# Kernel tuning notes

Hardware: AMD Instinct MI355X
Metric: run time of the kernel (lower is better)

Reference implementation:

```python
import jax, jax.numpy as jnp
import numpy as np

NEG_SLOPE = 0.2
EPS = 1e-16
HEADS1, OUT1 = 4, 32
HEADS2, OUT2 = 1, 32


def _gat_conv(x, W, a_src, a_dst, bias, src, dst, num_nodes, heads, out_c, concat):
    # x: [N, F_in], W: [F_in, heads*out_c], a_*: [heads, out_c]
    h = (x @ W).reshape(num_nodes, heads, out_c)            # [N, H, C]
    alpha_src = (h * a_src).sum(-1)                          # [N, H]
    alpha_dst = (h * a_dst).sum(-1)                          # [N, H]
    e = jax.nn.leaky_relu(alpha_src[src] + alpha_dst[dst], NEG_SLOPE)  # [E, H]
    # softmax over incoming edges of each destination node (PyG softmax)
    m = jax.ops.segment_max(e, dst, num_segments=num_nodes)
    ex = jnp.exp(e - m[dst])
    s = jax.ops.segment_sum(ex, dst, num_segments=num_nodes)
    alpha = ex / (s[dst] + EPS)                              # [E, H]
    out = jax.ops.segment_sum(h[src] * alpha[:, :, None], dst,
                              num_segments=num_nodes)        # [N, H, C]
    out = out.reshape(num_nodes, heads * out_c) if concat else out.mean(axis=1)
    return out + bias


def setup_inputs() -> dict:
    key = jax.random.key(0)
    ks = jax.random.split(key, 10)
    N, E, F_IN = 50000, 1600000, 128
    sc = 0.1
    return {
        "x": jax.random.normal(ks[0], (N, F_IN), jnp.float32),
        "edge_index": jax.random.randint(ks[1], (2, E), 0, N, jnp.int32),
        "W1": jax.random.normal(ks[2], (F_IN, HEADS1 * OUT1), jnp.float32) * sc,
        "a_src1": jax.random.normal(ks[3], (HEADS1, OUT1), jnp.float32) * sc,
        "a_dst1": jax.random.normal(ks[4], (HEADS1, OUT1), jnp.float32) * sc,
        "b1": jax.random.normal(ks[5], (HEADS1 * OUT1,), jnp.float32) * sc,
        "W2": jax.random.normal(ks[6], (HEADS1 * OUT1, HEADS2 * OUT2), jnp.float32) * sc,
        "a_src2": jax.random.normal(ks[7], (HEADS2, OUT2), jnp.float32) * sc,
        "a_dst2": jax.random.normal(ks[8], (HEADS2, OUT2), jnp.float32) * sc,
        "b2": jax.random.normal(ks[9], (OUT2,), jnp.float32) * sc,
    }


def reference(x, edge_index, W1, a_src1, a_dst1, b1, W2, a_src2, a_dst2, b2):
    N = x.shape[0]
    # PyG GATConv default add_self_loops=True
    loops = jnp.arange(N, dtype=edge_index.dtype)
    src = jnp.concatenate([edge_index[0], loops])
    dst = jnp.concatenate([edge_index[1], loops])
    h = _gat_conv(x, W1, a_src1, a_dst1, b1, src, dst, N, HEADS1, OUT1, True)
    h = jax.nn.elu(h)
    return _gat_conv(h, W2, a_src2, a_dst2, b2, src, dst, N, HEADS2, OUT2, False)
```

## Files before the change

### kernel.cpp

```cpp
#include <hip/hip_runtime.h>
#include <math.h>

#define NEG_SLOPE 0.2f
#define EPSV 1e-16f
#define NPART 16

typedef _Float16 half4 __attribute__((ext_vector_type(4)));
typedef _Float16 half8 __attribute__((ext_vector_type(8)));


__global__ void k_hist_rank(const int* __restrict__ ei, int E, int ET, int N,
                            int* __restrict__ degp, int* __restrict__ rank){
    int i = blockIdx.x * 256 + threadIdx.x;
    if (i < ET){
        int d = (i < E) ? ei[E + i] : (i - E);
        int p = blockIdx.x & (NPART - 1);
        rank[i] = atomicAdd(&degp[p * N + d], 1);
    }
}

__global__ void k_combine(const int* __restrict__ degp, int N,
                          int* __restrict__ deg, int* __restrict__ poff){
    int n = blockIdx.x * 256 + threadIdx.x;
    if (n < N){
        int s = 0;
        #pragma unroll
        for (int p = 0; p < NPART; p++){
            int t = degp[p * N + n];
            poff[p * N + n] = s;
            s += t;
        }
        deg[n] = s;
    }
}

__global__ void k_scan_blk(const int* __restrict__ deg, int N,
                           int* __restrict__ rowptr, int* __restrict__ bsum){
    int b = blockIdx.x, t = threadIdx.x;
    int base = b * 1024 + t * 4;
    int v[4];
    #pragma unroll
    for (int j = 0; j < 4; j++) v[j] = (base + j < N) ? deg[base + j] : 0;
    int s = v[0] + v[1] + v[2] + v[3];
    int lane = t & 63, wid = t >> 6;
    int x = s;
    #pragma unroll
    for (int off = 1; off < 64; off <<= 1){
        int y = __shfl_up(x, off, 64);
        if (lane >= off) x += y;
    }
    __shared__ int ws[4];
    if (lane == 63) ws[wid] = x;
    __syncthreads();
    int woff = 0;
    for (int w = 0; w < wid; w++) woff += ws[w];
    int run = woff + x - s;
    #pragma unroll
    for (int j = 0; j < 4; j++){
        if (base + j < N) rowptr[base + j] = run;
        run += v[j];
    }
    if (t == 255) bsum[b] = woff + x;
}

__global__ void k_scan_top(int* bsum, int nb){
    int t = threadIdx.x;
    int v = (t < nb) ? bsum[t] : 0;
    int x = v;
    #pragma unroll
    for (int off = 1; off < 64; off <<= 1){
        int y = __shfl_up(x, off, 64);
        if (t >= off) x += y;
    }
    if (t < nb) bsum[t] = x - v;
}

__global__ void k_finalize(const int* __restrict__ bsum, int N, int ET,
                           int* __restrict__ rowptr, int* __restrict__ poff){
    int n = blockIdx.x * 256 + threadIdx.x;
    if (n < N){
        int r = rowptr[n] + bsum[n >> 10];
        rowptr[n] = r;
        #pragma unroll
        for (int p = 0; p < NPART; p++) poff[p * N + n] += r;
    }
    if (n == 0) rowptr[N] = ET;
}

__launch_bounds__(256)
__global__ void k_scatter2(const int* __restrict__ ei, int E, int ET, int N,
                           const int* __restrict__ poff, const int* __restrict__ rank,
                           int* __restrict__ csr_src){
    int i = blockIdx.x * 256 + threadIdx.x;
    if (i >= ET) return;
    int s, d;
    if (i < E){ s = ei[i]; d = ei[E + i]; } else { s = i - E; d = s; }
    int p = blockIdx.x & (NPART - 1);
    csr_src[poff[p * N + d] + rank[i]] = s;
}


__launch_bounds__(256)
__global__ void k_gemm1(const float* __restrict__ x, const float* __restrict__ W1,
                        const float* __restrict__ a_src, const float* __restrict__ a_dst,
                        _Float16* __restrict__ h1h, float* __restrict__ asrc1,
                        float* __restrict__ adst1, int N){
    __shared__ float Wl[128 * 128];
    __shared__ float xl[32 * 128];
    int t = threadIdx.x;
    int cg = t & 31, ns = t >> 5;
    for (int idx = t; idx < 4096; idx += 256)
        *(float4*)&Wl[idx * 4] = *(const float4*)&W1[idx * 4];
    int n0 = blockIdx.x * 32;
    for (int idx = t; idx < 1024; idx += 256){
        int row = idx >> 5, k4 = idx & 31;
        float4 v = {0.f, 0.f, 0.f, 0.f};
        if (n0 + row < N) v = *(const float4*)&x[(size_t)(n0 + row) * 128 + k4 * 4];
        *(float4*)&xl[row * 128 + k4 * 4] = v;
    }
    __syncthreads();
    float4 acc0 = {0,0,0,0}, acc1 = {0,0,0,0}, acc2 = {0,0,0,0}, acc3 = {0,0,0,0};
    #pragma unroll 4
    for (int k = 0; k < 128; k++){
        float4 w = *(float4*)&Wl[k * 128 + cg * 4];
        float x0 = xl[(ns     ) * 128 + k];
        float x1 = xl[(ns +  8) * 128 + k];
        float x2v= xl[(ns + 16) * 128 + k];
        float x3 = xl[(ns + 24) * 128 + k];
        acc0.x = fmaf(x0, w.x, acc0.x); acc0.y = fmaf(x0, w.y, acc0.y);
        acc0.z = fmaf(x0, w.z, acc0.z); acc0.w = fmaf(x0, w.w, acc0.w);
        acc1.x = fmaf(x1, w.x, acc1.x); acc1.y = fmaf(x1, w.y, acc1.y);
        acc1.z = fmaf(x1, w.z, acc1.z); acc1.w = fmaf(x1, w.w, acc1.w);
        acc2.x = fmaf(x2v, w.x, acc2.x); acc2.y = fmaf(x2v, w.y, acc2.y);
        acc2.z = fmaf(x2v, w.z, acc2.z); acc2.w = fmaf(x2v, w.w, acc2.w);
        acc3.x = fmaf(x3, w.x, acc3.x); acc3.y = fmaf(x3, w.y, acc3.y);
        acc3.z = fmaf(x3, w.z, acc3.z); acc3.w = fmaf(x3, w.w, acc3.w);
    }
    float4 a4s = *(const float4*)&a_src[cg * 4];
    float4 a4d = *(const float4*)&a_dst[cg * 4];
    float4 accs[4] = {acc0, acc1, acc2, acc3};
    #pragma unroll
    for (int j = 0; j < 4; j++){
        int n = n0 + ns + 8 * j;
        if (n >= N) continue;
        float4 a = accs[j];
        half4 hv;
        hv.x = (_Float16)a.x; hv.y = (_Float16)a.y;
        hv.z = (_Float16)a.z; hv.w = (_Float16)a.w;
        *(half4*)&h1h[((size_t)n << 7) + (cg << 2)] = hv;
        float vs = a.x * a4s.x + a.y * a4s.y + a.z * a4s.z + a.w * a4s.w;
        float vd = a.x * a4d.x + a.y * a4d.y + a.z * a4d.z + a.w * a4d.w;
        #pragma unroll
        for (int m = 1; m <= 4; m <<= 1){
            vs += __shfl_xor(vs, m, 64);
            vd += __shfl_xor(vd, m, 64);
        }
        if ((cg & 7) == 0){
            int head = cg >> 3;
            asrc1[n * 4 + head] = vs;
            adst1[n * 4 + head] = vd;
        }
    }
}


__launch_bounds__(256)
__global__ void k_agg1(const int* __restrict__ rowptr, const int* __restrict__ csr_src,
                       const float* __restrict__ asrc1, const float* __restrict__ adst1,
                       const _Float16* __restrict__ h1h,
                       const float* __restrict__ b1, float* __restrict__ x2){
    int t = threadIdx.x;
    int n = blockIdx.x * 4 + (t >> 6);
    int lane = t & 63, g = lane >> 4, l = lane & 15, head = l >> 2;
    int start = rowptr[n], end = rowptr[n + 1];
    float adn = adst1[(n << 2) + head];
    float rA[8] = {0,0,0,0,0,0,0,0}, rB[8] = {0,0,0,0,0,0,0,0};
    float sA = 0.f, sB = 0.f;
    int i = start + g;
    for (; i + 4 < end; i += 8){
        int s0 = csr_src[i];
        int s1 = csr_src[i + 4];
        float e0 = asrc1[(s0 << 2) + head] + adn;
        float e1 = asrc1[(s1 << 2) + head] + adn;
        e0 = fmaxf(e0, NEG_SLOPE * e0);
        e1 = fmaxf(e1, NEG_SLOPE * e1);
        float w0 = __expf(e0);
        float w1 = __expf(e1);
        half8 h0 = *(const half8*)&h1h[((size_t)s0 << 7) + (l << 3)];
        half8 h1v = *(const half8*)&h1h[((size_t)s1 << 7) + (l << 3)];
        sA += w0; sB += w1;
        #pragma unroll
        for (int j = 0; j < 8; j++){
            rA[j] = fmaf(w0, (float)h0[j], rA[j]);
            rB[j] = fmaf(w1, (float)h1v[j], rB[j]);
        }
    }
    if (i < end){
        int s0 = csr_src[i];
        float e0 = asrc1[(s0 << 2) + head] + adn;
        e0 = fmaxf(e0, NEG_SLOPE * e0);
        float w0 = __expf(e0);
        half8 h0 = *(const half8*)&h1h[((size_t)s0 << 7) + (l << 3)];
        sA += w0;
        #pragma unroll
        for (int j = 0; j < 8; j++) rA[j] = fmaf(w0, (float)h0[j], rA[j]);
    }
    float r[9];
    #pragma unroll
    for (int j = 0; j < 8; j++) r[j] = rA[j] + rB[j];
    r[8] = sA + sB;
    #pragma unroll
    for (int m = 16; m <= 32; m <<= 1)
        #pragma unroll
        for (int j = 0; j < 9; j++) r[j] += __shfl_xor(r[j], m, 64);
    if (g == 0){
        float inv = 1.f / (r[8] + EPSV);
        float o[8];
        #pragma unroll
        for (int j = 0; j < 8; j++){
            float v = r[j] * inv + b1[l * 8 + j];
            o[j] = (v > 0.f) ? v : expm1f(v);
        }
        float4 o0 = {o[0], o[1], o[2], o[3]};
        float4 o1 = {o[4], o[5], o[6], o[7]};
        *(float4*)&x2[((size_t)n << 7) + (l << 3)]     = o0;
        *(float4*)&x2[((size_t)n << 7) + (l << 3) + 4] = o1;
    }
}


__launch_bounds__(256)
__global__ void k_gemm2(const float* __restrict__ x2, const float* __restrict__ W2,
                        const float* __restrict__ a_src, const float* __restrict__ a_dst,
                        _Float16* __restrict__ h2h, float* __restrict__ asrc2,
                        float* __restrict__ adst2, int N){
    __shared__ float Wl[128 * 32];
    __shared__ float xl[128 * 128];
    int t = threadIdx.x;
    int cg = t & 7, ns = t >> 3;
    for (int idx = t; idx < 1024; idx += 256)
        *(float4*)&Wl[idx * 4] = *(const float4*)&W2[idx * 4];
    int n0 = blockIdx.x * 128;
    for (int idx = t; idx < 4096; idx += 256){
        int row = idx >> 5, k4 = idx & 31;
        float4 v = {0.f, 0.f, 0.f, 0.f};
        if (n0 + row < N) v = *(const float4*)&x2[(size_t)(n0 + row) * 128 + k4 * 4];
        *(float4*)&xl[row * 128 + k4 * 4] = v;
    }
    __syncthreads();
    float4 acc0 = {0,0,0,0}, acc1 = {0,0,0,0}, acc2 = {0,0,0,0}, acc3 = {0,0,0,0};
    #pragma unroll 4
    for (int k = 0; k < 128; k++){
        float4 w = *(float4*)&Wl[k * 32 + cg * 4];
        float x0 = xl[(ns      ) * 128 + k];
        float x1 = xl[(ns +  32) * 128 + k];
        float x2v= xl[(ns +  64) * 128 + k];
        float x3 = xl[(ns +  96) * 128 + k];
        acc0.x = fmaf(x0, w.x, acc0.x); acc0.y = fmaf(x0, w.y, acc0.y);
        acc0.z = fmaf(x0, w.z, acc0.z); acc0.w = fmaf(x0, w.w, acc0.w);
        acc1.x = fmaf(x1, w.x, acc1.x); acc1.y = fmaf(x1, w.y, acc1.y);
        acc1.z = fmaf(x1, w.z, acc1.z); acc1.w = fmaf(x1, w.w, acc1.w);
        acc2.x = fmaf(x2v, w.x, acc2.x); acc2.y = fmaf(x2v, w.y, acc2.y);
        acc2.z = fmaf(x2v, w.z, acc2.z); acc2.w = fmaf(x2v, w.w, acc2.w);
        acc3.x = fmaf(x3, w.x, acc3.x); acc3.y = fmaf(x3, w.y, acc3.y);
        acc3.z = fmaf(x3, w.z, acc3.z); acc3.w = fmaf(x3, w.w, acc3.w);
    }
    float4 a4s = *(const float4*)&a_src[cg * 4];
    float4 a4d = *(const float4*)&a_dst[cg * 4];
    float4 accs[4] = {acc0, acc1, acc2, acc3};
    #pragma unroll
    for (int j = 0; j < 4; j++){
        int n = n0 + ns + 32 * j;
        if (n >= N) continue;
        float4 a = accs[j];
        half4 hv;
        hv.x = (_Float16)a.x; hv.y = (_Float16)a.y;
        hv.z = (_Float16)a.z; hv.w = (_Float16)a.w;
        *(half4*)&h2h[((size_t)n << 5) + (cg << 2)] = hv;
        float vs = a.x * a4s.x + a.y * a4s.y + a.z * a4s.z + a.w * a4s.w;
        float vd = a.x * a4d.x + a.y * a4d.y + a.z * a4d.z + a.w * a4d.w;
        #pragma unroll
        for (int m = 1; m <= 4; m <<= 1){
            vs += __shfl_xor(vs, m, 64);
            vd += __shfl_xor(vd, m, 64);
        }
        if (cg == 0){ asrc2[n] = vs; adst2[n] = vd; }
    }
}


__launch_bounds__(256)
__global__ void k_agg2(const int* __restrict__ rowptr, const int* __restrict__ csr_src,
                       const float* __restrict__ asrc2, const float* __restrict__ adst2,
                       const _Float16* __restrict__ h2h,
                       const float* __restrict__ b2, float* __restrict__ out){
    int t = threadIdx.x;
    int n = blockIdx.x * 4 + (t >> 6);
    int lane = t & 63, g = lane >> 3, l = lane & 7;
    int start = rowptr[n], end = rowptr[n + 1];
    float adn = adst2[n];
    float4 aA = {0,0,0,0}, aB = {0,0,0,0};
    float sA = 0.f, sB = 0.f;
    int i = start + g;
    for (; i + 8 < end; i += 16){
        int s0 = csr_src[i];
        int s1 = csr_src[i + 8];
        float e0 = asrc2[s0] + adn;
        float e1 = asrc2[s1] + adn;
        e0 = fmaxf(e0, NEG_SLOPE * e0);
        e1 = fmaxf(e1, NEG_SLOPE * e1);
        float w0 = __expf(e0);
        float w1 = __expf(e1);
        half4 h0 = *(const half4*)&h2h[((size_t)s0 << 5) + (l << 2)];
        half4 h1v = *(const half4*)&h2h[((size_t)s1 << 5) + (l << 2)];
        sA += w0; sB += w1;
        aA.x = fmaf(w0, (float)h0.x, aA.x); aA.y = fmaf(w0, (float)h0.y, aA.y);
        aA.z = fmaf(w0, (float)h0.z, aA.z); aA.w = fmaf(w0, (float)h0.w, aA.w);
        aB.x = fmaf(w1, (float)h1v.x, aB.x); aB.y = fmaf(w1, (float)h1v.y, aB.y);
        aB.z = fmaf(w1, (float)h1v.z, aB.z); aB.w = fmaf(w1, (float)h1v.w, aB.w);
    }
    if (i < end){
        int s0 = csr_src[i];
        float e0 = asrc2[s0] + adn;
        e0 = fmaxf(e0, NEG_SLOPE * e0);
        float w0 = __expf(e0);
        half4 h0 = *(const half4*)&h2h[((size_t)s0 << 5) + (l << 2)];
        sA += w0;
        aA.x = fmaf(w0, (float)h0.x, aA.x); aA.y = fmaf(w0, (float)h0.y, aA.y);
        aA.z = fmaf(w0, (float)h0.z, aA.z); aA.w = fmaf(w0, (float)h0.w, aA.w);
    }
    float4 acc = {aA.x + aB.x, aA.y + aB.y, aA.z + aB.z, aA.w + aB.w};
    float ssum = sA + sB;
    #pragma unroll
    for (int m = 8; m <= 32; m <<= 1){
        acc.x += __shfl_xor(acc.x, m, 64);
        acc.y += __shfl_xor(acc.y, m, 64);
        acc.z += __shfl_xor(acc.z, m, 64);
        acc.w += __shfl_xor(acc.w, m, 64);
        ssum  += __shfl_xor(ssum,  m, 64);
    }
    if (g == 0){
        float inv = 1.f / (ssum + EPSV);
        const float4 b4 = *(const float4*)&b2[l * 4];
        float4 o;
        o.x = acc.x * inv + b4.x; o.y = acc.y * inv + b4.y;
        o.z = acc.z * inv + b4.z; o.w = acc.w * inv + b4.w;
        *(float4*)&out[((size_t)n << 5) + l * 4] = o;
    }
}


extern "C" void kernel_launch(void* const* d_in, const int* in_sizes, int n_in,
                              void* d_out, int out_size, void* d_ws, size_t ws_size,
                              hipStream_t stream){
    const float* x      = (const float*)d_in[0];
    const int*   ei     = (const int*)  d_in[1];
    const float* W1     = (const float*)d_in[2];
    const float* a_src1 = (const float*)d_in[3];
    const float* a_dst1 = (const float*)d_in[4];
    const float* b1     = (const float*)d_in[5];
    const float* W2     = (const float*)d_in[6];
    const float* a_src2 = (const float*)d_in[7];
    const float* a_dst2 = (const float*)d_in[8];
    const float* b2     = (const float*)d_in[9];
    float* out = (float*)d_out;

    int N  = in_sizes[0] / 128;
    int E  = in_sizes[1] / 2;
    int ET = E + N;
    int nScanBlk = (N + 1023) / 1024;
    int G  = (ET + 255) / 256;

    char* ws = (char*)d_ws;
    size_t off = 0;
    auto alloc = [&](size_t bytes) -> char* {
        char* p = ws + off;
        off += (bytes + 255) & ~(size_t)255;
        return p;
    };
    int*      degp    = (int*)     alloc((size_t)NPART * N * 4);
    int*      deg     = (int*)     alloc((size_t)N * 4);
    int*      rowptr  = (int*)     alloc((size_t)(N + 1) * 4);
    int*      bsum    = (int*)     alloc((size_t)nScanBlk * 4);
    int*      rank    = (int*)     alloc((size_t)ET * 4);
    int*      poff    = (int*)     alloc((size_t)NPART * N * 4);
    int*      csr_src = (int*)     alloc((size_t)ET * 4);
    _Float16* h1h     = (_Float16*)alloc((size_t)N * 128 * 2);
    float*    x2      = (float*)   alloc((size_t)N * 128 * 4);
    float*    asrc1   = (float*)   alloc((size_t)N * 4 * 4);
    float*    adst1   = (float*)   alloc((size_t)N * 4 * 4);
    _Float16* h2h     = (_Float16*)alloc((size_t)N * 32 * 2);
    float*    asrc2   = (float*)   alloc((size_t)N * 4);
    float*    adst2   = (float*)   alloc((size_t)N * 4);

    hipMemsetAsync(degp, 0, (size_t)NPART * N * 4, stream);
    hipLaunchKernelGGL(k_hist_rank, dim3(G), dim3(256), 0, stream, ei, E, ET, N, degp, rank);
    hipLaunchKernelGGL(k_combine,   dim3((N + 255) / 256), dim3(256), 0, stream, degp, N, deg, poff);
    hipLaunchKernelGGL(k_scan_blk,  dim3(nScanBlk), dim3(256), 0, stream, deg, N, rowptr, bsum);
    hipLaunchKernelGGL(k_scan_top,  dim3(1),        dim3(64),  0, stream, bsum, nScanBlk);
    hipLaunchKernelGGL(k_finalize,  dim3((N + 255) / 256), dim3(256), 0, stream, bsum, N, ET, rowptr, poff);
    hipLaunchKernelGGL(k_scatter2,  dim3(G), dim3(256), 0, stream, ei, E, ET, N, poff, rank, csr_src);
    hipLaunchKernelGGL(k_gemm1,     dim3((N + 31) / 32), dim3(256), 0, stream, x, W1, a_src1, a_dst1, h1h, asrc1, adst1, N);
    hipLaunchKernelGGL(k_agg1,      dim3(N / 4), dim3(256), 0, stream, rowptr, csr_src, asrc1, adst1, h1h, b1, x2);
    hipLaunchKernelGGL(k_gemm2,     dim3((N + 127) / 128), dim3(256), 0, stream, x2, W2, a_src2, a_dst2, h2h, asrc2, adst2, N);
    hipLaunchKernelGGL(k_agg2,      dim3(N / 4), dim3(256), 0, stream, rowptr, csr_src, asrc2, adst2, h2h, b2, out);
}
```

Before: 343.4 us.

## Fold CSR scan kernels, vectorize GEMM x loads, deepen aggregation unroll

Merges k_combine and k_scan_top into the scan and finalize kernels, so finalize now recomputes the block-sum prefix and the per-partition offsets directly from degp. This removes two launches and the intermediate deg buffer. Both GEMM inner loops now read x from shared memory as float4 instead of as scalars. Both aggregation kernels now use four independent accumulator streams instead of two, giving more memory-level parallelism on the gathers. The cost is more register pressure and some redundant reads of bsum and degp.

```diff
diff --git a/kernel.cpp b/kernel.cpp
--- a/kernel.cpp
+++ b/kernel.cpp
@@ -19,28 +19,20 @@
     }
 }
 
-__global__ void k_combine(const int* __restrict__ degp, int N,
-                          int* __restrict__ deg, int* __restrict__ poff){
-    int n = blockIdx.x * 256 + threadIdx.x;
-    if (n < N){
-        int s = 0;
-        #pragma unroll
-        for (int p = 0; p < NPART; p++){
-            int t = degp[p * N + n];
-            poff[p * N + n] = s;
-            s += t;
-        }
-        deg[n] = s;
-    }
-}
-
-__global__ void k_scan_blk(const int* __restrict__ deg, int N,
+__global__ void k_scan_blk(const int* __restrict__ degp, int N,
                            int* __restrict__ rowptr, int* __restrict__ bsum){
     int b = blockIdx.x, t = threadIdx.x;
     int base = b * 1024 + t * 4;
     int v[4];
     #pragma unroll
-    for (int j = 0; j < 4; j++) v[j] = (base + j < N) ? deg[base + j] : 0;
+    for (int j = 0; j < 4; j++){
+        int n = base + j, s = 0;
+        if (n < N){
+            #pragma unroll
+            for (int p = 0; p < NPART; p++) s += degp[p * N + n];
+        }
+        v[j] = s;
+    }
     int s = v[0] + v[1] + v[2] + v[3];
     int lane = t & 63, wid = t >> 6;
     int x = s;
@@ -63,26 +55,23 @@
     if (t == 255) bsum[b] = woff + x;
 }
 
-__global__ void k_scan_top(int* bsum, int nb){
-    int t = threadIdx.x;
-    int v = (t < nb) ? bsum[t] : 0;
-    int x = v;
-    #pragma unroll
-    for (int off = 1; off < 64; off <<= 1){
-        int y = __shfl_up(x, off, 64);
-        if (t >= off) x += y;
-    }
-    if (t < nb) bsum[t] = x - v;
-}
-
-__global__ void k_finalize(const int* __restrict__ bsum, int N, int ET,
+__global__ void k_finalize(const int* __restrict__ bsum, const int* __restrict__ degp,
+                           int N, int ET,
                            int* __restrict__ rowptr, int* __restrict__ poff){
-    int n = blockIdx.x * 256 + threadIdx.x;
+    int b = blockIdx.x, t = threadIdx.x;
+    int n = b * 256 + t;
+    int chunk = (b * 256) >> 10;
+    int off = 0;
+    for (int c = 0; c < chunk; c++) off += bsum[c];
     if (n < N){
-        int r = rowptr[n] + bsum[n >> 10];
+        int r = rowptr[n] + off;
         rowptr[n] = r;
-        #pragma unroll
-        for (int p = 0; p < NPART; p++) poff[p * N + n] += r;
+        int run = r;
+        #pragma unroll
+        for (int p = 0; p < NPART; p++){
+            poff[p * N + n] = run;
+            run += degp[p * N + n];
+        }
     }
     if (n == 0) rowptr[N] = ET;
 }
@@ -120,21 +109,28 @@
     }
     __syncthreads();
     float4 acc0 = {0,0,0,0}, acc1 = {0,0,0,0}, acc2 = {0,0,0,0}, acc3 = {0,0,0,0};
-    #pragma unroll 4
-    for (int k = 0; k < 128; k++){
-        float4 w = *(float4*)&Wl[k * 128 + cg * 4];
-        float x0 = xl[(ns     ) * 128 + k];
-        float x1 = xl[(ns +  8) * 128 + k];
-        float x2v= xl[(ns + 16) * 128 + k];
-        float x3 = xl[(ns + 24) * 128 + k];
-        acc0.x = fmaf(x0, w.x, acc0.x); acc0.y = fmaf(x0, w.y, acc0.y);
-        acc0.z = fmaf(x0, w.z, acc0.z); acc0.w = fmaf(x0, w.w, acc0.w);
-        acc1.x = fmaf(x1, w.x, acc1.x); acc1.y = fmaf(x1, w.y, acc1.y);
-        acc1.z = fmaf(x1, w.z, acc1.z); acc1.w = fmaf(x1, w.w, acc1.w);
-        acc2.x = fmaf(x2v, w.x, acc2.x); acc2.y = fmaf(x2v, w.y, acc2.y);
-        acc2.z = fmaf(x2v, w.z, acc2.z); acc2.w = fmaf(x2v, w.w, acc2.w);
-        acc3.x = fmaf(x3, w.x, acc3.x); acc3.y = fmaf(x3, w.y, acc3.y);
-        acc3.z = fmaf(x3, w.z, acc3.z); acc3.w = fmaf(x3, w.w, acc3.w);
+    #pragma unroll 2
+    for (int k = 0; k < 128; k += 4){
+        float4 xv0 = *(float4*)&xl[(ns     ) * 128 + k];
+        float4 xv1 = *(float4*)&xl[(ns +  8) * 128 + k];
+        float4 xv2 = *(float4*)&xl[(ns + 16) * 128 + k];
+        float4 xv3 = *(float4*)&xl[(ns + 24) * 128 + k];
+        #pragma unroll
+        for (int kk = 0; kk < 4; kk++){
+            float4 w = *(float4*)&Wl[(k + kk) * 128 + cg * 4];
+            float x0 = ((float*)&xv0)[kk];
+            float x1 = ((float*)&xv1)[kk];
+            float x2v= ((float*)&xv2)[kk];
+            float x3 = ((float*)&xv3)[kk];
+            acc0.x = fmaf(x0, w.x, acc0.x); acc0.y = fmaf(x0, w.y, acc0.y);
+            acc0.z = fmaf(x0, w.z, acc0.z); acc0.w = fmaf(x0, w.w, acc0.w);
+            acc1.x = fmaf(x1, w.x, acc1.x); acc1.y = fmaf(x1, w.y, acc1.y);
+            acc1.z = fmaf(x1, w.z, acc1.z); acc1.w = fmaf(x1, w.w, acc1.w);
+            acc2.x = fmaf(x2v, w.x, acc2.x); acc2.y = fmaf(x2v, w.y, acc2.y);
+            acc2.z = fmaf(x2v, w.z, acc2.z); acc2.w = fmaf(x2v, w.w, acc2.w);
+            acc3.x = fmaf(x3, w.x, acc3.x); acc3.y = fmaf(x3, w.y, acc3.y);
+            acc3.z = fmaf(x3, w.z, acc3.z); acc3.w = fmaf(x3, w.w, acc3.w);
+        }
     }
     float4 a4s = *(const float4*)&a_src[cg * 4];
     float4 a4d = *(const float4*)&a_dst[cg * 4];
@@ -175,27 +171,35 @@
     int start = rowptr[n], end = rowptr[n + 1];
     float adn = adst1[(n << 2) + head];
     float rA[8] = {0,0,0,0,0,0,0,0}, rB[8] = {0,0,0,0,0,0,0,0};
-    float sA = 0.f, sB = 0.f;
+    float rC[8] = {0,0,0,0,0,0,0,0}, rD[8] = {0,0,0,0,0,0,0,0};
+    float sA = 0.f, sB = 0.f, sC = 0.f, sD = 0.f;
     int i = start + g;
-    for (; i + 4 < end; i += 8){
+    for (; i + 12 < end; i += 16){
         int s0 = csr_src[i];
         int s1 = csr_src[i + 4];
+        int s2 = csr_src[i + 8];
+        int s3 = csr_src[i + 12];
         float e0 = asrc1[(s0 << 2) + head] + adn;
         float e1 = asrc1[(s1 << 2) + head] + adn;
-        e0 = fmaxf(e0, NEG_SLOPE * e0);
-        e1 = fmaxf(e1, NEG_SLOPE * e1);
-        float w0 = __expf(e0);
-        float w1 = __expf(e1);
+        float e2 = asrc1[(s2 << 2) + head] + adn;
+        float e3 = asrc1[(s3 << 2) + head] + adn;
+        e0 = fmaxf(e0, NEG_SLOPE * e0); e1 = fmaxf(e1, NEG_SLOPE * e1);
+        e2 = fmaxf(e2, NEG_SLOPE * e2); e3 = fmaxf(e3, NEG_SLOPE * e3);
+        float w0 = __expf(e0), w1 = __expf(e1), w2 = __expf(e2), w3 = __expf(e3);
         half8 h0 = *(const half8*)&h1h[((size_t)s0 << 7) + (l << 3)];
         half8 h1v = *(const half8*)&h1h[((size_t)s1 << 7) + (l << 3)];
-        sA += w0; sB += w1;
+        half8 h2v = *(const half8*)&h1h[((size_t)s2 << 7) + (l << 3)];
+        half8 h3v = *(const half8*)&h1h[((size_t)s3 << 7) + (l << 3)];
+        sA += w0; sB += w1; sC += w2; sD += w3;
         #pragma unroll
         for (int j = 0; j < 8; j++){
             rA[j] = fmaf(w0, (float)h0[j], rA[j]);
             rB[j] = fmaf(w1, (float)h1v[j], rB[j]);
-        }
-    }
-    if (i < end){
+            rC[j] = fmaf(w2, (float)h2v[j], rC[j]);
+            rD[j] = fmaf(w3, (float)h3v[j], rD[j]);
+        }
+    }
+    for (; i < end; i += 4){
         int s0 = csr_src[i];
         float e0 = asrc1[(s0 << 2) + head] + adn;
         e0 = fmaxf(e0, NEG_SLOPE * e0);
@@ -207,8 +211,8 @@
     }
     float r[9];
     #pragma unroll
-    for (int j = 0; j < 8; j++) r[j] = rA[j] + rB[j];
-    r[8] = sA + sB;
+    for (int j = 0; j < 8; j++) r[j] = (rA[j] + rB[j]) + (rC[j] + rD[j]);
+    r[8] = (sA + sB) + (sC + sD);
     #pragma unroll
     for (int m = 16; m <= 32; m <<= 1)
         #pragma unroll
@@ -249,21 +253,28 @@
     }
     __syncthreads();
     float4 acc0 = {0,0,0,0}, acc1 = {0,0,0,0}, acc2 = {0,0,0,0}, acc3 = {0,0,0,0};
-    #pragma unroll 4
-    for (int k = 0; k < 128; k++){
-        float4 w = *(float4*)&Wl[k * 32 + cg * 4];
-        float x0 = xl[(ns      ) * 128 + k];
-        float x1 = xl[(ns +  32) * 128 + k];
-        float x2v= xl[(ns +  64) * 128 + k];
-        float x3 = xl[(ns +  96) * 128 + k];
-        acc0.x = fmaf(x0, w.x, acc0.x); acc0.y = fmaf(x0, w.y, acc0.y);
-        acc0.z = fmaf(x0, w.z, acc0.z); acc0.w = fmaf(x0, w.w, acc0.w);
-        acc1.x = fmaf(x1, w.x, acc1.x); acc1.y = fmaf(x1, w.y, acc1.y);
-        acc1.z = fmaf(x1, w.z, acc1.z); acc1.w = fmaf(x1, w.w, acc1.w);
-        acc2.x = fmaf(x2v, w.x, acc2.x); acc2.y = fmaf(x2v, w.y, acc2.y);
-        acc2.z = fmaf(x2v, w.z, acc2.z); acc2.w = fmaf(x2v, w.w, acc2.w);
-        acc3.x = fmaf(x3, w.x, acc3.x); acc3.y = fmaf(x3, w.y, acc3.y);
-        acc3.z = fmaf(x3, w.z, acc3.z); acc3.w = fmaf(x3, w.w, acc3.w);
+    #pragma unroll 2
+    for (int k = 0; k < 128; k += 4){
+        float4 xv0 = *(float4*)&xl[(ns      ) * 128 + k];
+        float4 xv1 = *(float4*)&xl[(ns +  32) * 128 + k];
+        float4 xv2 = *(float4*)&xl[(ns +  64) * 128 + k];
+        float4 xv3 = *(float4*)&xl[(ns +  96) * 128 + k];
+        #pragma unroll
+        for (int kk = 0; kk < 4; kk++){
+            float4 w = *(float4*)&Wl[(k + kk) * 32 + cg * 4];
+            float x0 = ((float*)&xv0)[kk];
+            float x1 = ((float*)&xv1)[kk];
+            float x2v= ((float*)&xv2)[kk];
+            float x3 = ((float*)&xv3)[kk];
+            acc0.x = fmaf(x0, w.x, acc0.x); acc0.y = fmaf(x0, w.y, acc0.y);
+            acc0.z = fmaf(x0, w.z, acc0.z); acc0.w = fmaf(x0, w.w, acc0.w);
+            acc1.x = fmaf(x1, w.x, acc1.x); acc1.y = fmaf(x1, w.y, acc1.y);
+            acc1.z = fmaf(x1, w.z, acc1.z); acc1.w = fmaf(x1, w.w, acc1.w);
+            acc2.x = fmaf(x2v, w.x, acc2.x); acc2.y = fmaf(x2v, w.y, acc2.y);
+            acc2.z = fmaf(x2v, w.z, acc2.z); acc2.w = fmaf(x2v, w.w, acc2.w);
+            acc3.x = fmaf(x3, w.x, acc3.x); acc3.y = fmaf(x3, w.y, acc3.y);
+            acc3.z = fmaf(x3, w.z, acc3.z); acc3.w = fmaf(x3, w.w, acc3.w);
+        }
     }
     float4 a4s = *(const float4*)&a_src[cg * 4];
     float4 a4d = *(const float4*)&a_dst[cg * 4];
@@ -299,27 +310,34 @@
     int lane = t & 63, g = lane >> 3, l = lane & 7;
     int start = rowptr[n], end = rowptr[n + 1];
     float adn = adst2[n];
-    float4 aA = {0,0,0,0}, aB = {0,0,0,0};
-    float sA = 0.f, sB = 0.f;
+    float4 aA = {0,0,0,0}, aB = {0,0,0,0}, aC = {0,0,0,0}, aD = {0,0,0,0};
+    float sA = 0.f, sB = 0.f, sC = 0.f, sD = 0.f;
     int i = start + g;
-    for (; i + 8 < end; i += 16){
+    for (; i + 24 < end; i += 32){
         int s0 = csr_src[i];
         int s1 = csr_src[i + 8];
-        float e0 = asrc2[s0] + adn;
-        float e1 = asrc2[s1] + adn;
-        e0 = fmaxf(e0, NEG_SLOPE * e0);
-        e1 = fmaxf(e1, NEG_SLOPE * e1);
-        float w0 = __expf(e0);
-        float w1 = __expf(e1);
+        int s2 = csr_src[i + 16];
+        int s3 = csr_src[i + 24];
+        float e0 = asrc2[s0] + adn, e1 = asrc2[s1] + adn;
+        float e2 = asrc2[s2] + adn, e3 = asrc2[s3] + adn;
+        e0 = fmaxf(e0, NEG_SLOPE * e0); e1 = fmaxf(e1, NEG_SLOPE * e1);
+        e2 = fmaxf(e2, NEG_SLOPE * e2); e3 = fmaxf(e3, NEG_SLOPE * e3);
+        float w0 = __expf(e0), w1 = __expf(e1), w2 = __expf(e2), w3 = __expf(e3);
         half4 h0 = *(const half4*)&h2h[((size_t)s0 << 5) + (l << 2)];
         half4 h1v = *(const half4*)&h2h[((size_t)s1 << 5) + (l << 2)];
-        sA += w0; sB += w1;
+        half4 h2v = *(const half4*)&h2h[((size_t)s2 << 5) + (l << 2)];
+        half4 h3v = *(const half4*)&h2h[((size_t)s3 << 5) + (l << 2)];
+        sA += w0; sB += w1; sC += w2; sD += w3;
         aA.x = fmaf(w0, (float)h0.x, aA.x); aA.y = fmaf(w0, (float)h0.y, aA.y);
         aA.z = fmaf(w0, (float)h0.z, aA.z); aA.w = fmaf(w0, (float)h0.w, aA.w);
         aB.x = fmaf(w1, (float)h1v.x, aB.x); aB.y = fmaf(w1, (float)h1v.y, aB.y);
         aB.z = fmaf(w1, (float)h1v.z, aB.z); aB.w = fmaf(w1, (float)h1v.w, aB.w);
-    }
-    if (i < end){
+        aC.x = fmaf(w2, (float)h2v.x, aC.x); aC.y = fmaf(w2, (float)h2v.y, aC.y);
+        aC.z = fmaf(w2, (float)h2v.z, aC.z); aC.w = fmaf(w2, (float)h2v.w, aC.w);
+        aD.x = fmaf(w3, (float)h3v.x, aD.x); aD.y = fmaf(w3, (float)h3v.y, aD.y);
+        aD.z = fmaf(w3, (float)h3v.z, aD.z); aD.w = fmaf(w3, (float)h3v.w, aD.w);
+    }
+    for (; i < end; i += 8){
         int s0 = csr_src[i];
         float e0 = asrc2[s0] + adn;
         e0 = fmaxf(e0, NEG_SLOPE * e0);
@@ -329,8 +347,9 @@
         aA.x = fmaf(w0, (float)h0.x, aA.x); aA.y = fmaf(w0, (float)h0.y, aA.y);
         aA.z = fmaf(w0, (float)h0.z, aA.z); aA.w = fmaf(w0, (float)h0.w, aA.w);
     }
-    float4 acc = {aA.x + aB.x, aA.y + aB.y, aA.z + aB.z, aA.w + aB.w};
-    float ssum = sA + sB;
+    float4 acc = {(aA.x + aB.x) + (aC.x + aD.x), (aA.y + aB.y) + (aC.y + aD.y),
+                  (aA.z + aB.z) + (aC.z + aD.z), (aA.w + aB.w) + (aC.w + aD.w)};
+    float ssum = (sA + sB) + (sC + sD);
     #pragma unroll
     for (int m = 8; m <= 32; m <<= 1){
         acc.x += __shfl_xor(acc.x, m, 64);
@@ -379,7 +398,6 @@
         return p;
     };
     int*      degp    = (int*)     alloc((size_t)NPART * N * 4);
-    int*      deg     = (int*)     alloc((size_t)N * 4);
     int*      rowptr  = (int*)     alloc((size_t)(N + 1) * 4);
     int*      bsum    = (int*)     alloc((size_t)nScanBlk * 4);
     int*      rank    = (int*)     alloc((size_t)ET * 4);
@@ -395,10 +413,8 @@
 
     hipMemsetAsync(degp, 0, (size_t)NPART * N * 4, stream);
     hipLaunchKernelGGL(k_hist_rank, dim3(G), dim3(256), 0, stream, ei, E, ET, N, degp, rank);
-    hipLaunchKernelGGL(k_combine,   dim3((N + 255) / 256), dim3(256), 0, stream, degp, N, deg, poff);
-    hipLaunchKernelGGL(k_scan_blk,  dim3(nScanBlk), dim3(256), 0, stream, deg, N, rowptr, bsum);
-    hipLaunchKernelGGL(k_scan_top,  dim3(1),        dim3(64),  0, stream, bsum, nScanBlk);
-    hipLaunchKernelGGL(k_finalize,  dim3((N + 255) / 256), dim3(256), 0, stream, bsum, N, ET, rowptr, poff);
+    hipLaunchKernelGGL(k_scan_blk,  dim3(nScanBlk), dim3(256), 0, stream, degp, N, rowptr, bsum);
+    hipLaunchKernelGGL(k_finalize,  dim3((N + 255) / 256), dim3(256), 0, stream, bsum, degp, N, ET, rowptr, poff);
     hipLaunchKernelGGL(k_scatter2,  dim3(G), dim3(256), 0, stream, ei, E, ET, N, poff, rank, csr_src);
     hipLaunchKernelGGL(k_gemm1,     dim3((N + 31) / 32), dim3(256), 0, stream, x, W1, a_src1, a_dst1, h1h, asrc1, adst1, N);
     hipLaunchKernelGGL(k_agg1,      dim3(N / 4), dim3(256), 0, stream, rowptr, csr_src, asrc1, adst1, h1h, b1, x2);
```

New measurement: 354.5 us. 3.2% more time.
